# Optimization experiments

Hardware: AMD Instinct MI355X
Metric: run time of the kernel (lower is better)

The kernel has to match this reference:

```python
import jax, jax.numpy as jnp
import numpy as np

H = 12      # num attention heads
W = 128     # one-sided window size (band = 2W+1), also the chunk size
G = 32      # number of global tokens (positions 0..G-1)
NEG = -1e9


def setup_inputs() -> dict:
    key = jax.random.key(0)
    ks = jax.random.split(key, 9)
    B, S, D = 1, 4096, 768
    std = 0.02
    f32 = jnp.float32
    return {
        "hidden_states": jax.random.normal(ks[0], (B, S, D), f32),
        "Wq": jax.random.normal(ks[1], (D, D), f32) * std,
        "bq": jnp.zeros((D,), f32),
        "Wk": jax.random.normal(ks[2], (D, D), f32) * std,
        "bk": jnp.zeros((D,), f32),
        "Wv": jax.random.normal(ks[3], (D, D), f32) * std,
        "bv": jnp.zeros((D,), f32),
        "Wo": jax.random.normal(ks[4], (D, D), f32) * std,
        "bo": jnp.zeros((D,), f32),
    }


def _longformer_attn(hidden, Wq, bq, Wk, bk, Wv, bv, Wo, bo):
    B, S, D = hidden.shape
    dh = D // H
    scale = jnp.asarray(dh, hidden.dtype) ** -0.5

    def proj(Wm, bm):
        return (hidden @ Wm + bm).reshape(B, S, H, dh).transpose(0, 2, 1, 3)  # [B,H,S,dh]

    q = proj(Wq, bq) * scale
    k = proj(Wk, bk)
    v = proj(Wv, bv)

    nc = S // W  # number of query chunks
    q_ch = q.reshape(B, H, nc, W, dh)

    # pad keys/values by one chunk on each side; chunk c sees keys [c*W - W, c*W + 2W)
    kp = jnp.pad(k, ((0, 0), (0, 0), (W, W), (0, 0)))
    vp = jnp.pad(v, ((0, 0), (0, 0), (W, W), (0, 0)))
    idx = (jnp.arange(nc) * W)[:, None] + jnp.arange(3 * W)[None, :]  # [nc, 3W] into padded seq
    k_ch = kp[:, :, idx]  # [B,H,nc,3W,dh]
    v_ch = vp[:, :, idx]

    # banded scores via chunked matmul: [B,H,nc,W,3W]
    band = jnp.einsum('bhcqd,bhckd->bhcqk', q_ch, k_ch)

    # exact band mask |i-j| <= W: with local query qi and local key kj (global j = c*W + kj - W)
    qi = jnp.arange(W)[:, None]           # [W,1]
    kj = jnp.arange(3 * W)[None, :]       # [1,3W]
    in_band = (kj >= qi) & (kj <= qi + 2 * W)                     # [W,3W]
    j = (jnp.arange(nc) * W)[:, None, None] + kj[None] - W        # [nc,1,3W] global key index
    valid = in_band[None] & (j >= G) & (j < S)                    # [nc,W,3W]; j<G handled via global path
    band = jnp.where(valid[None, None], band, NEG)
    band = band.reshape(B, H, S, 3 * W)

    # every query also attends to the G global keys
    gsc = jnp.einsum('bhsd,bhgd->bhsg', q, k[:, :, :G])           # [B,H,S,G]
    scores = jnp.concatenate([gsc, band], axis=-1)                # [B,H,S,G+3W]
    probs = jax.nn.softmax(scores, axis=-1)

    out = jnp.einsum('bhsg,bhgd->bhsd', probs[..., :G], v[:, :, :G])
    pb = probs[..., G:].reshape(B, H, nc, W, 3 * W)
    out = out + jnp.einsum('bhcqk,bhckd->bhcqd', pb, v_ch).reshape(B, H, S, dh)

    # global queries attend to everything (full attention on G rows)
    gq_probs = jax.nn.softmax(jnp.einsum('bhgd,bhsd->bhgs', q[:, :, :G], k), axis=-1)
    out_g = jnp.einsum('bhgs,bhsd->bhgd', gq_probs, v)
    out = out.at[:, :, :G].set(out_g)

    out = out.transpose(0, 2, 1, 3).reshape(B, S, D)
    return out @ Wo + bo


def reference(hidden_states, Wq, bq, Wk, bk, Wv, bv, Wo, bo):
    return _longformer_attn(hidden_states, Wq, bq, Wk, bk, Wv, bv, Wo, bo)
```

## Files before the change

### kernel.cpp

```cpp
#include <hip/hip_runtime.h>
#include <stdint.h>

#define S_LEN 4096
#define DMOD  768
#define NH    12
#define DH    64
#define GG    32
#define NEGBIG (-1e9f)

typedef _Float16 f16;
typedef f16 f16x8 __attribute__((ext_vector_type(8)));
typedef f16 f16x4 __attribute__((ext_vector_type(4)));
typedef float f32x4 __attribute__((ext_vector_type(4)));
typedef uint32_t u32;

#define OFF_H16   ((size_t)0)
#define OFF_WT    ((size_t)6291456)
#define OFF_Q     ((size_t)11010048)
#define OFF_K     ((size_t)17301504)
#define OFF_VT    ((size_t)29884416)
#define OFF_ATT   ((size_t)36175872)
#define OFF_GQO   ((size_t)42467328)
#define OFF_GQL   ((size_t)44040192)

__device__ __forceinline__ void gld_lds16(const void* g, void* l) {
  typedef __attribute__((address_space(3))) u32 lds_u32;
  typedef __attribute__((address_space(1))) u32 glb_u32;
  __builtin_amdgcn_global_load_lds((glb_u32*)(uintptr_t)g,
                                   (lds_u32*)(u32)(uintptr_t)l, 16, 0, 0);
}

__global__ __launch_bounds__(256) void prep_kernel(
    const float* __restrict__ hs,
    const float* __restrict__ Wq, const float* __restrict__ Wk,
    const float* __restrict__ Wv, const float* __restrict__ Wo,
    f16* __restrict__ h16, f16* __restrict__ wt)
{
  const int b = blockIdx.x;
  const int t = threadIdx.x;
  if (b < 576) {
    __shared__ float tile[64][65];
    const int w = b / 144, r2 = b % 144;
    const int n0 = (r2 % 12) * 64, k0 = (r2 / 12) * 64;
    const float* W = (w==0) ? Wq : (w==1) ? Wk : (w==2) ? Wv : Wo;
    f16* WT = wt + (size_t)w * DMOD * DMOD;
    #pragma unroll
    for (int rnd = 0; rnd < 4; ++rnd) {
      const int lin = rnd * 1024 + t * 4;
      const int r = lin >> 6, c = lin & 63;
      const float4 vv = *(const float4*)(W + (size_t)(k0 + r) * DMOD + n0 + c);
      tile[r][c+0] = vv.x; tile[r][c+1] = vv.y; tile[r][c+2] = vv.z; tile[r][c+3] = vv.w;
    }
    __syncthreads();
    #pragma unroll
    for (int rnd = 0; rnd < 2; ++rnd) {
      const int lin = rnd * 256 + t;
      const int n = lin >> 3, kc = (lin & 7) * 8;
      f16x8 o;
      #pragma unroll
      for (int j = 0; j < 8; ++j) o[j] = (f16)tile[kc + j][n];
      *(f16x8*)(WT + (size_t)(n0 + n) * DMOD + k0 + kc) = o;
    }
  } else {
    const size_t idx = (size_t)(b - 576) * 2048 + (size_t)t * 8;
    const float4 a = *(const float4*)(hs + idx);
    const float4 c = *(const float4*)(hs + idx + 4);
    f16x8 o;
    o[0]=(f16)a.x; o[1]=(f16)a.y; o[2]=(f16)a.z; o[3]=(f16)a.w;
    o[4]=(f16)c.x; o[5]=(f16)c.y; o[6]=(f16)c.z; o[7]=(f16)c.w;
    *(f16x8*)(h16 + idx) = o;
  }
}

__global__ __launch_bounds__(256) void gemm_qkv(
    const f16* __restrict__ A, const f16* __restrict__ wt,
    const float* __restrict__ bq, const float* __restrict__ bk, const float* __restrict__ bv,
    f16* __restrict__ q16, f16* __restrict__ k16, f16* __restrict__ vt16)
{
  __shared__ __align__(16) f16 At[3][4096];
  __shared__ __align__(16) f16 Bt[3][4096];
  const int z = blockIdx.z;
  const f16* Wt = wt + (size_t)z * DMOD * DMOD;
  const float* bias = (z==0) ? bq : (z==1) ? bk : bv;
  const float scale = (z==0) ? 0.125f : 1.0f;

  const int tid = threadIdx.x;
  const int lane = tid & 63, wid = tid >> 6;
  const int quad = lane >> 4, l15 = lane & 15;
  const int n0 = blockIdx.x * 128, m0 = blockIdx.y * 128;
  const int wm = (wid >> 1) * 64, wn = (wid & 1) * 64;

  f32x4 acc[4][4];
  #pragma unroll
  for (int i=0;i<4;++i)
    #pragma unroll
    for (int j=0;j<4;++j) acc[i][j] = (f32x4){0.f,0.f,0.f,0.f};

  const int lin0 = tid, lin1 = tid + 256;
  const int ar0 = ((lin0>>6)<<4) + (lin0&15), ac0 = ((lin0>>4)&3)*8;
  const int ar1 = ((lin1>>6)<<4) + (lin1&15), ac1 = ((lin1>>4)&3)*8;
  const f16* Ab = A  + (size_t)m0 * DMOD;
  const f16* Bb = Wt + (size_t)n0 * DMOD;

  gld_lds16(Ab + (size_t)ar0*DMOD + ac0, &At[0][lin0*8]);
  gld_lds16(Ab + (size_t)ar1*DMOD + ac1, &At[0][lin1*8]);
  gld_lds16(Bb + (size_t)ar0*DMOD + ac0, &Bt[0][lin0*8]);
  gld_lds16(Bb + (size_t)ar1*DMOD + ac1, &Bt[0][lin1*8]);

  int cur = 0;
  #pragma unroll 3
  for (int k = 0; k < 24; ++k) {
    const int nxt = (cur == 2) ? 0 : cur + 1;
    if (k < 23) {
      const int k0 = (k + 1) * 32;
      gld_lds16(Ab + (size_t)ar0*DMOD + k0 + ac0, &At[nxt][lin0*8]);
      gld_lds16(Ab + (size_t)ar1*DMOD + k0 + ac1, &At[nxt][lin1*8]);
      gld_lds16(Bb + (size_t)ar0*DMOD + k0 + ac0, &Bt[nxt][lin0*8]);
      gld_lds16(Bb + (size_t)ar1*DMOD + k0 + ac1, &Bt[nxt][lin1*8]);
      asm volatile("s_waitcnt vmcnt(4) lgkmcnt(0)" ::: "memory");
    } else {
      asm volatile("s_waitcnt vmcnt(0) lgkmcnt(0)" ::: "memory");
    }
    __builtin_amdgcn_s_barrier();
    f16x8 af[4], bf[4];
    #pragma unroll
    for (int i=0;i<4;++i) {
      af[i] = *(const f16x8*)(&At[cur][((wm>>4)+i)*512 + lane*8]);
      bf[i] = *(const f16x8*)(&Bt[cur][((wn>>4)+i)*512 + lane*8]);
    }
    #pragma unroll
    for (int i=0;i<4;++i)
      #pragma unroll
      for (int j=0;j<4;++j)
        acc[i][j] = __builtin_amdgcn_mfma_f32_16x16x32_f16(af[i], bf[j], acc[i][j], 0, 0, 0);
    cur = nxt;
  }

  if (z < 2) {
    f16* outp = (z==0) ? q16 : k16;
    #pragma unroll
    for (int j=0;j<4;++j) {
      const int col = n0 + wn + j*16 + l15;
      const float bcol = bias[col];
      const int h = col >> 6, d = col & 63;
      #pragma unroll
      for (int i=0;i<4;++i) {
        const int rbase = m0 + wm + i*16 + quad*4;
        f16* dst = outp + ((size_t)h * S_LEN + rbase) * DH + d;
        #pragma unroll
        for (int r=0;r<4;++r)
          dst[(size_t)r * DH] = (f16)((acc[i][j][r] + bcol) * scale);
      }
    }
  } else {
    #pragma unroll
    for (int j=0;j<4;++j) {
      const int col = n0 + wn + j*16 + l15;
      const float bcol = bias[col];
      const int h = col >> 6, d = col & 63;
      #pragma unroll
      for (int i=0;i<4;++i) {
        const int rbase = m0 + wm + i*16 + quad*4;
        f16x4 o;
        #pragma unroll
        for (int r=0;r<4;++r) o[r] = (f16)(acc[i][j][r] + bcol);
        *(f16x4*)(vt16 + ((size_t)h * DH + d) * S_LEN + rbase) = o;
      }
    }
  }
}

__global__ __launch_bounds__(256) void gemm_out(
    const f16* __restrict__ A, const f16* __restrict__ Wt,
    const float* __restrict__ bo, float* __restrict__ outp)
{
  __shared__ __align__(16) f16 At[3][4096];
  __shared__ __align__(16) f16 Bt[3][2048];
  const int tid = threadIdx.x;
  const int lane = tid & 63, wid = tid >> 6;
  const int quad = lane >> 4, l15 = lane & 15;
  const int n0 = blockIdx.x * 64, m0 = blockIdx.y * 128;
  const int wm = (wid >> 1) * 64, wn = (wid & 1) * 32;

  f32x4 acc[4][2];
  #pragma unroll
  for (int i=0;i<4;++i)
    #pragma unroll
    for (int j=0;j<2;++j) acc[i][j] = (f32x4){0.f,0.f,0.f,0.f};

  const int lin0 = tid, lin1 = tid + 256;
  const int ar0 = ((lin0>>6)<<4) + (lin0&15), ac0 = ((lin0>>4)&3)*8;
  const int ar1 = ((lin1>>6)<<4) + (lin1&15), ac1 = ((lin1>>4)&3)*8;
  const f16* Ab = A  + (size_t)m0 * DMOD;
  const f16* Bb = Wt + (size_t)n0 * DMOD;

  gld_lds16(Ab + (size_t)ar0*DMOD + ac0, &At[0][lin0*8]);
  gld_lds16(Ab + (size_t)ar1*DMOD + ac1, &At[0][lin1*8]);
  gld_lds16(Bb + (size_t)ar0*DMOD + ac0, &Bt[0][lin0*8]);

  int cur = 0;
  #pragma unroll 3
  for (int k = 0; k < 24; ++k) {
    const int nxt = (cur == 2) ? 0 : cur + 1;
    if (k < 23) {
      const int k0 = (k + 1) * 32;
      gld_lds16(Ab + (size_t)ar0*DMOD + k0 + ac0, &At[nxt][lin0*8]);
      gld_lds16(Ab + (size_t)ar1*DMOD + k0 + ac1, &At[nxt][lin1*8]);
      gld_lds16(Bb + (size_t)ar0*DMOD + k0 + ac0, &Bt[nxt][lin0*8]);
      asm volatile("s_waitcnt vmcnt(3) lgkmcnt(0)" ::: "memory");
    } else {
      asm volatile("s_waitcnt vmcnt(0) lgkmcnt(0)" ::: "memory");
    }
    __builtin_amdgcn_s_barrier();
    f16x8 af[4], bf[2];
    #pragma unroll
    for (int i=0;i<4;++i)
      af[i] = *(const f16x8*)(&At[cur][((wm>>4)+i)*512 + lane*8]);
    #pragma unroll
    for (int j=0;j<2;++j)
      bf[j] = *(const f16x8*)(&Bt[cur][((wn>>4)+j)*512 + lane*8]);
    #pragma unroll
    for (int i=0;i<4;++i)
      #pragma unroll
      for (int j=0;j<2;++j)
        acc[i][j] = __builtin_amdgcn_mfma_f32_16x16x32_f16(af[i], bf[j], acc[i][j], 0, 0, 0);
    cur = nxt;
  }

  #pragma unroll
  for (int j=0;j<2;++j) {
    const int col = n0 + wn + j*16 + l15;
    const float bcol = bo[col];
    #pragma unroll
    for (int i=0;i<4;++i) {
      const int rbase = m0 + wm + i*16 + quad*4;
      #pragma unroll
      for (int r=0;r<4;++r)
        outp[(size_t)(rbase + r) * DMOD + col] = acc[i][j][r] + bcol;
    }
  }
}

__global__ __launch_bounds__(256) void band_attn(
    const f16* __restrict__ q16, const f16* __restrict__ k16,
    const f16* __restrict__ vt16, f16* __restrict__ att16,
    float* __restrict__ o_part, float* __restrict__ l_part)
{
  __shared__ __align__(16) f16 Pbuf[4][1280];
  const int h = blockIdx.y;
  const int tid = threadIdx.x, lane = tid & 63, wid = tid >> 6;
  const int quad = lane >> 4, l15 = lane & 15;
  f16* P = &Pbuf[wid][0];

  const int bx = blockIdx.x;
  const bool is_gq = (bx >= 32);
  int gr0 = 0, sp = 0, tcount;
  if (is_gq) {
    sp = (bx - 32) * 4 + wid;
    tcount = 8;
  } else {
    const int sub = bx * 4 + wid;
    if (sub == 0) return;
    gr0 = sub * 32;
    tcount = 10;
  }

  const f16* qh = q16 + (size_t)h * S_LEN * DH;
  const f16* kh = k16 + (size_t)h * S_LEN * DH;
  const f16* vh = vt16 + (size_t)h * DH * S_LEN;

  f16x8 aq[2][2];
  #pragma unroll
  for (int mt=0;mt<2;++mt)
    #pragma unroll
    for (int ks=0;ks<2;++ks)
      aq[mt][ks] = *(const f16x8*)(qh + (size_t)(gr0 + mt*16 + l15)*DH + ks*32 + quad*8);

  f32x4 accO[2][4];
  float lacc[2][4];
  #pragma unroll
  for (int mt=0;mt<2;++mt) {
    #pragma unroll
    for (int n=0;n<4;++n) accO[mt][n] = (f32x4){0.f,0.f,0.f,0.f};
    #pragma unroll
    for (int r=0;r<4;++r) lacc[mt][r] = 0.f;
  }

  for (int t = 0; t < tcount; ++t) {
    int j0;
    if (is_gq) {
      j0 = sp*256 + t*32;
    } else if (t > 0) {
      j0 = gr0 - 128 + (t-1)*32;
      if (j0 <= 0 || j0 >= S_LEN) continue;
    } else {
      j0 = 0;
    }
    f16x8 bk[2][2];
    #pragma unroll
    for (int nt=0;nt<2;++nt) {
      const int key = j0 + nt*16 + l15;
      #pragma unroll
      for (int ks=0;ks<2;++ks)
        bk[nt][ks] = *(const f16x8*)(kh + (size_t)key*DH + ks*32 + quad*8);
    }
    f32x4 sc[2][2];
    #pragma unroll
    for (int mt=0;mt<2;++mt)
      #pragma unroll
      for (int nt=0;nt<2;++nt) {
        f32x4 s = __builtin_amdgcn_mfma_f32_16x16x32_f16(aq[mt][0], bk[nt][0],
                                                         (f32x4){0.f,0.f,0.f,0.f}, 0,0,0);
        sc[mt][nt] = __builtin_amdgcn_mfma_f32_16x16x32_f16(aq[mt][1], bk[nt][1], s, 0,0,0);
      }
    if (!is_gq && (t == 1 || t == 9)) {
      #pragma unroll
      for (int nt=0;nt<2;++nt)
        #pragma unroll
        for (int mt=0;mt<2;++mt)
          #pragma unroll
          for (int r=0;r<4;++r) {
            const int e = (nt*16 + l15) - (mt*16 + quad*4 + r);
            const bool ok = (t == 1) ? (e >= 0) : (e <= 0);
            if (!ok) sc[mt][nt][r] = NEGBIG;
          }
    }
    #pragma unroll
    for (int mt=0;mt<2;++mt)
      #pragma unroll
      for (int r=0;r<4;++r) {
        sc[mt][0][r] = __expf(sc[mt][0][r]);
        sc[mt][1][r] = __expf(sc[mt][1][r]);
        lacc[mt][r] += sc[mt][0][r] + sc[mt][1][r];
      }
    #pragma unroll
    for (int mt=0;mt<2;++mt)
      #pragma unroll
      for (int nt=0;nt<2;++nt)
        #pragma unroll
        for (int r=0;r<4;++r)
          P[(mt*16 + quad*4 + r)*40 + nt*16 + l15] = (f16)sc[mt][nt][r];
    asm volatile("s_waitcnt lgkmcnt(0)" ::: "memory");
    f16x8 ap[2];
    #pragma unroll
    for (int mt=0;mt<2;++mt)
      ap[mt] = *(const f16x8*)(P + (mt*16 + l15)*40 + quad*8);
    #pragma unroll
    for (int n=0;n<4;++n) {
      const f16x8 bv = *(const f16x8*)(vh + (size_t)(n*16 + l15)*S_LEN + j0 + quad*8);
      #pragma unroll
      for (int mt=0;mt<2;++mt)
        accO[mt][n] = __builtin_amdgcn_mfma_f32_16x16x32_f16(ap[mt], bv, accO[mt][n], 0,0,0);
    }
  }

  #pragma unroll
  for (int mt=0;mt<2;++mt)
    #pragma unroll
    for (int r=0;r<4;++r) {
      float v = lacc[mt][r];
      v += __shfl_xor(v, 1, 64);
      v += __shfl_xor(v, 2, 64);
      v += __shfl_xor(v, 4, 64);
      v += __shfl_xor(v, 8, 64);
      lacc[mt][r] = v;
    }

  if (is_gq) {
    const int base = (h*16 + sp)*32;
    #pragma unroll
    for (int mt=0;mt<2;++mt)
      #pragma unroll
      for (int r=0;r<4;++r) {
        const int row = mt*16 + quad*4 + r;
        if (l15 == 0) l_part[base+row] = lacc[mt][r];
        #pragma unroll
        for (int n=0;n<4;++n)
          o_part[(size_t)(base+row)*DH + n*16 + l15] = accO[mt][n][r];
      }
  } else {
    #pragma unroll
    for (int mt=0;mt<2;++mt)
      #pragma unroll
      for (int r=0;r<4;++r) {
        const float inv = 1.f / lacc[mt][r];
        const int s = gr0 + mt*16 + quad*4 + r;
        #pragma unroll
        for (int n=0;n<4;++n)
          att16[(size_t)s * DMOD + h*DH + n*16 + l15] = (f16)(accO[mt][n][r] * inv);
      }
  }
}

__global__ __launch_bounds__(256) void gq_merge(
    const float* __restrict__ o_part, const float* __restrict__ l_part,
    f16* __restrict__ att16)
{
  const int h = blockIdx.x;
  const int t = threadIdx.x;
  for (int u = t; u < 512; u += 256) {
    const int row = u >> 4, c4 = u & 15;
    float4 s = {0.f,0.f,0.f,0.f};
    float l = 0.f;
    for (int sp=0;sp<16;++sp) {
      const int base = (h*16 + sp)*32 + row;
      const float4 v = *(const float4*)&o_part[(size_t)base*DH + c4*4];
      s.x += v.x; s.y += v.y; s.z += v.z; s.w += v.w;
      l += l_part[base];
    }
    const float inv = 1.f / l;
    f16x4 o;
    o[0] = (f16)(s.x*inv); o[1] = (f16)(s.y*inv);
    o[2] = (f16)(s.z*inv); o[3] = (f16)(s.w*inv);
    *(f16x4*)&att16[(size_t)row * DMOD + h*DH + c4*4] = o;
  }
}

extern "C" void kernel_launch(void* const* d_in, const int* in_sizes, int n_in,
                              void* d_out, int out_size, void* d_ws, size_t ws_size,
                              hipStream_t stream)
{
  const float* hs = (const float*)d_in[0];
  const float* Wq = (const float*)d_in[1];
  const float* bq = (const float*)d_in[2];
  const float* Wk = (const float*)d_in[3];
  const float* bk = (const float*)d_in[4];
  const float* Wv = (const float*)d_in[5];
  const float* bv = (const float*)d_in[6];
  const float* Wo = (const float*)d_in[7];
  const float* bo = (const float*)d_in[8];
  float* out = (float*)d_out;
  char* ws = (char*)d_ws;
  f16* h16  = (f16*)(ws + OFF_H16);
  f16* wt   = (f16*)(ws + OFF_WT);
  f16* q16  = (f16*)(ws + OFF_Q);
  f16* k16  = (f16*)(ws + OFF_K);
  f16* vt16 = (f16*)(ws + OFF_VT);
  f16* att16= (f16*)(ws + OFF_ATT);
  float* gqo = (float*)(ws + OFF_GQO);
  float* gql = (float*)(ws + OFF_GQL);

  prep_kernel<<<2112, 256, 0, stream>>>(hs, Wq, Wk, Wv, Wo, h16, wt);
  gemm_qkv<<<dim3(6,32,3), 256, 0, stream>>>(h16, wt, bq, bk, bv, q16, k16, vt16);
  band_attn<<<dim3(36,12), 256, 0, stream>>>(q16, k16, vt16, att16, gqo, gql);
  gq_merge<<<12, 256, 0, stream>>>(gqo, gql, att16);
  gemm_out<<<dim3(12,32), 256, 0, stream>>>(att16, wt + (size_t)3*DMOD*DMOD, bo, out);
}
```

Before: 170.7 us.

## Halve GEMM M-tile and prefetch two stages ahead in QKV and output GEMMs

Reduces the M tile of both projection GEMMs from 128 to 64 rows, doubling the grid so more blocks fill the CUs. The triple-buffered LDS pipeline now issues loads two k-steps ahead, after the barrier, with adjusted waitcnt values. Smaller tiles lower per-block data reuse and raise global/L2 traffic for weights in exchange for better occupancy and latency hiding.

```diff
diff --git a/kernel.cpp b/kernel.cpp
--- a/kernel.cpp
+++ b/kernel.cpp
@@ -77,7 +77,7 @@
     const float* __restrict__ bq, const float* __restrict__ bk, const float* __restrict__ bv,
     f16* __restrict__ q16, f16* __restrict__ k16, f16* __restrict__ vt16)
 {
-  __shared__ __align__(16) f16 At[3][4096];
+  __shared__ __align__(16) f16 At[3][2048];
   __shared__ __align__(16) f16 Bt[3][4096];
   const int z = blockIdx.z;
   const f16* Wt = wt + (size_t)z * DMOD * DMOD;
@@ -87,53 +87,57 @@
   const int tid = threadIdx.x;
   const int lane = tid & 63, wid = tid >> 6;
   const int quad = lane >> 4, l15 = lane & 15;
-  const int n0 = blockIdx.x * 128, m0 = blockIdx.y * 128;
-  const int wm = (wid >> 1) * 64, wn = (wid & 1) * 64;
-
-  f32x4 acc[4][4];
-  #pragma unroll
-  for (int i=0;i<4;++i)
+  const int n0 = blockIdx.x * 128, m0 = blockIdx.y * 64;
+  const int wm = (wid >> 1) * 32, wn = (wid & 1) * 64;
+
+  f32x4 acc[2][4];
+  #pragma unroll
+  for (int i=0;i<2;++i)
     #pragma unroll
     for (int j=0;j<4;++j) acc[i][j] = (f32x4){0.f,0.f,0.f,0.f};
 
-  const int lin0 = tid, lin1 = tid + 256;
-  const int ar0 = ((lin0>>6)<<4) + (lin0&15), ac0 = ((lin0>>4)&3)*8;
-  const int ar1 = ((lin1>>6)<<4) + (lin1&15), ac1 = ((lin1>>4)&3)*8;
+  const int arA = ((tid>>6)<<4) + (tid&15), acA = ((tid>>4)&3)*8;
+  const int b0 = tid, b1 = tid + 256;
+  const int arB0 = ((b0>>6)<<4) + (b0&15), acB0 = ((b0>>4)&3)*8;
+  const int arB1 = ((b1>>6)<<4) + (b1&15), acB1 = ((b1>>4)&3)*8;
   const f16* Ab = A  + (size_t)m0 * DMOD;
   const f16* Bb = Wt + (size_t)n0 * DMOD;
 
-  gld_lds16(Ab + (size_t)ar0*DMOD + ac0, &At[0][lin0*8]);
-  gld_lds16(Ab + (size_t)ar1*DMOD + ac1, &At[0][lin1*8]);
-  gld_lds16(Bb + (size_t)ar0*DMOD + ac0, &Bt[0][lin0*8]);
-  gld_lds16(Bb + (size_t)ar1*DMOD + ac1, &Bt[0][lin1*8]);
-
-  int cur = 0;
+  #pragma unroll
+  for (int p = 0; p < 2; ++p) {
+    const int k0 = p * 32;
+    gld_lds16(Ab + (size_t)arA*DMOD  + k0 + acA,  &At[p][tid*8]);
+    gld_lds16(Bb + (size_t)arB0*DMOD + k0 + acB0, &Bt[p][b0*8]);
+    gld_lds16(Bb + (size_t)arB1*DMOD + k0 + acB1, &Bt[p][b1*8]);
+  }
+
   #pragma unroll 3
   for (int k = 0; k < 24; ++k) {
-    const int nxt = (cur == 2) ? 0 : cur + 1;
+    const int cb = k % 3, ib = (k + 2) % 3;
     if (k < 23) {
-      const int k0 = (k + 1) * 32;
-      gld_lds16(Ab + (size_t)ar0*DMOD + k0 + ac0, &At[nxt][lin0*8]);
-      gld_lds16(Ab + (size_t)ar1*DMOD + k0 + ac1, &At[nxt][lin1*8]);
-      gld_lds16(Bb + (size_t)ar0*DMOD + k0 + ac0, &Bt[nxt][lin0*8]);
-      gld_lds16(Bb + (size_t)ar1*DMOD + k0 + ac1, &Bt[nxt][lin1*8]);
-      asm volatile("s_waitcnt vmcnt(4) lgkmcnt(0)" ::: "memory");
+      asm volatile("s_waitcnt vmcnt(3) lgkmcnt(0)" ::: "memory");
     } else {
       asm volatile("s_waitcnt vmcnt(0) lgkmcnt(0)" ::: "memory");
     }
     __builtin_amdgcn_s_barrier();
-    f16x8 af[4], bf[4];
-    #pragma unroll
-    for (int i=0;i<4;++i) {
-      af[i] = *(const f16x8*)(&At[cur][((wm>>4)+i)*512 + lane*8]);
-      bf[i] = *(const f16x8*)(&Bt[cur][((wn>>4)+i)*512 + lane*8]);
-    }
-    #pragma unroll
-    for (int i=0;i<4;++i)
+    if (k < 22) {
+      const int k0 = (k + 2) * 32;
+      gld_lds16(Ab + (size_t)arA*DMOD  + k0 + acA,  &At[ib][tid*8]);
+      gld_lds16(Bb + (size_t)arB0*DMOD + k0 + acB0, &Bt[ib][b0*8]);
+      gld_lds16(Bb + (size_t)arB1*DMOD + k0 + acB1, &Bt[ib][b1*8]);
+    }
+    f16x8 af[2], bf[4];
+    #pragma unroll
+    for (int i=0;i<2;++i)
+      af[i] = *(const f16x8*)(&At[cb][((wm>>4)+i)*512 + lane*8]);
+    #pragma unroll
+    for (int j=0;j<4;++j)
+      bf[j] = *(const f16x8*)(&Bt[cb][((wn>>4)+j)*512 + lane*8]);
+    #pragma unroll
+    for (int i=0;i<2;++i)
       #pragma unroll
       for (int j=0;j<4;++j)
         acc[i][j] = __builtin_amdgcn_mfma_f32_16x16x32_f16(af[i], bf[j], acc[i][j], 0, 0, 0);
-    cur = nxt;
   }
 
   if (z < 2) {
@@ -144,7 +148,7 @@
       const float bcol = bias[col];
       const int h = col >> 6, d = col & 63;
       #pragma unroll
-      for (int i=0;i<4;++i) {
+      for (int i=0;i<2;++i) {
         const int rbase = m0 + wm + i*16 + quad*4;
         f16* dst = outp + ((size_t)h * S_LEN + rbase) * DH + d;
         #pragma unroll
@@ -159,7 +163,7 @@
       const float bcol = bias[col];
       const int h = col >> 6, d = col & 63;
       #pragma unroll
-      for (int i=0;i<4;++i) {
+      for (int i=0;i<2;++i) {
         const int rbase = m0 + wm + i*16 + quad*4;
         f16x4 o;
         #pragma unroll
@@ -174,57 +178,56 @@
     const f16* __restrict__ A, const f16* __restrict__ Wt,
     const float* __restrict__ bo, float* __restrict__ outp)
 {
-  __shared__ __align__(16) f16 At[3][4096];
+  __shared__ __align__(16) f16 At[3][2048];
   __shared__ __align__(16) f16 Bt[3][2048];
   const int tid = threadIdx.x;
   const int lane = tid & 63, wid = tid >> 6;
   const int quad = lane >> 4, l15 = lane & 15;
-  const int n0 = blockIdx.x * 64, m0 = blockIdx.y * 128;
-  const int wm = (wid >> 1) * 64, wn = (wid & 1) * 32;
-
-  f32x4 acc[4][2];
-  #pragma unroll
-  for (int i=0;i<4;++i)
+  const int n0 = blockIdx.x * 64, m0 = blockIdx.y * 64;
+  const int wm = (wid >> 1) * 32, wn = (wid & 1) * 32;
+
+  f32x4 acc[2][2];
+  #pragma unroll
+  for (int i=0;i<2;++i)
     #pragma unroll
     for (int j=0;j<2;++j) acc[i][j] = (f32x4){0.f,0.f,0.f,0.f};
 
-  const int lin0 = tid, lin1 = tid + 256;
-  const int ar0 = ((lin0>>6)<<4) + (lin0&15), ac0 = ((lin0>>4)&3)*8;
-  const int ar1 = ((lin1>>6)<<4) + (lin1&15), ac1 = ((lin1>>4)&3)*8;
+  const int ar = ((tid>>6)<<4) + (tid&15), ac = ((tid>>4)&3)*8;
   const f16* Ab = A  + (size_t)m0 * DMOD;
   const f16* Bb = Wt + (size_t)n0 * DMOD;
 
-  gld_lds16(Ab + (size_t)ar0*DMOD + ac0, &At[0][lin0*8]);
-  gld_lds16(Ab + (size_t)ar1*DMOD + ac1, &At[0][lin1*8]);
-  gld_lds16(Bb + (size_t)ar0*DMOD + ac0, &Bt[0][lin0*8]);
-
-  int cur = 0;
+  #pragma unroll
+  for (int p = 0; p < 2; ++p) {
+    const int k0 = p * 32;
+    gld_lds16(Ab + (size_t)ar*DMOD + k0 + ac, &At[p][tid*8]);
+    gld_lds16(Bb + (size_t)ar*DMOD + k0 + ac, &Bt[p][tid*8]);
+  }
+
   #pragma unroll 3
   for (int k = 0; k < 24; ++k) {
-    const int nxt = (cur == 2) ? 0 : cur + 1;
+    const int cb = k % 3, ib = (k + 2) % 3;
     if (k < 23) {
-      const int k0 = (k + 1) * 32;
-      gld_lds16(Ab + (size_t)ar0*DMOD + k0 + ac0, &At[nxt][lin0*8]);
-      gld_lds16(Ab + (size_t)ar1*DMOD + k0 + ac1, &At[nxt][lin1*8]);
-      gld_lds16(Bb + (size_t)ar0*DMOD + k0 + ac0, &Bt[nxt][lin0*8]);
-      asm volatile("s_waitcnt vmcnt(3) lgkmcnt(0)" ::: "memory");
+      asm volatile("s_waitcnt vmcnt(2) lgkmcnt(0)" ::: "memory");
     } else {
       asm volatile("s_waitcnt vmcnt(0) lgkmcnt(0)" ::: "memory");
     }
     __builtin_amdgcn_s_barrier();
-    f16x8 af[4], bf[2];
-    #pragma unroll
-    for (int i=0;i<4;++i)
-      af[i] = *(const f16x8*)(&At[cur][((wm>>4)+i)*512 + lane*8]);
-    #pragma unroll
-    for (int j=0;j<2;++j)
-      bf[j] = *(const f16x8*)(&Bt[cur][((wn>>4)+j)*512 + lane*8]);
-    #pragma unroll
-    for (int i=0;i<4;++i)
+    if (k < 22) {
+      const int k0 = (k + 2) * 32;
+      gld_lds16(Ab + (size_t)ar*DMOD + k0 + ac, &At[ib][tid*8]);
+      gld_lds16(Bb + (size_t)ar*DMOD + k0 + ac, &Bt[ib][tid*8]);
+    }
+    f16x8 af[2], bf[2];
+    #pragma unroll
+    for (int i=0;i<2;++i) {
+      af[i] = *(const f16x8*)(&At[cb][((wm>>4)+i)*512 + lane*8]);
+      bf[i] = *(const f16x8*)(&Bt[cb][((wn>>4)+i)*512 + lane*8]);
+    }
+    #pragma unroll
+    for (int i=0;i<2;++i)
       #pragma unroll
       for (int j=0;j<2;++j)
         acc[i][j] = __builtin_amdgcn_mfma_f32_16x16x32_f16(af[i], bf[j], acc[i][j], 0, 0, 0);
-    cur = nxt;
   }
 
   #pragma unroll
@@ -232,7 +235,7 @@
     const int col = n0 + wn + j*16 + l15;
     const float bcol = bo[col];
     #pragma unroll
-    for (int i=0;i<4;++i) {
+    for (int i=0;i<2;++i) {
       const int rbase = m0 + wm + i*16 + quad*4;
       #pragma unroll
       for (int r=0;r<4;++r)
@@ -441,8 +444,8 @@
   float* gql = (float*)(ws + OFF_GQL);
 
   prep_kernel<<<2112, 256, 0, stream>>>(hs, Wq, Wk, Wv, Wo, h16, wt);
-  gemm_qkv<<<dim3(6,32,3), 256, 0, stream>>>(h16, wt, bq, bk, bv, q16, k16, vt16);
+  gemm_qkv<<<dim3(6,64,3), 256, 0, stream>>>(h16, wt, bq, bk, bv, q16, k16, vt16);
   band_attn<<<dim3(36,12), 256, 0, stream>>>(q16, k16, vt16, att16, gqo, gql);
   gq_merge<<<12, 256, 0, stream>>>(gqo, gql, att16);
-  gemm_out<<<dim3(12,32), 256, 0, stream>>>(att16, wt + (size_t)3*DMOD*DMOD, bo, out);
-}
+  gemm_out<<<dim3(12,64), 256, 0, stream>>>(att16, wt + (size_t)3*DMOD*DMOD, bo, out);
+}
```

Result: slower. 177.0 us (+3.7%).
